# Optimization experiments

Measured on AMD Instinct MI355X. Metric: run time of the kernel, lower is better.

## Reference

```python
import jax, jax.numpy as jnp
import numpy as np

D_MODEL = 1024
N_HEADS = 16
D_HEAD = 64
D_MLP = 4096
EPS = 1e-6


def setup_inputs() -> dict:
    key = jax.random.key(0)
    ks = jax.random.split(key, 12)
    s = lambda fan_in: 1.0 / np.sqrt(fan_in)
    x = jax.random.normal(ks[0], (2, 2048, D_MODEL), dtype=jnp.float32)
    inp = {
        "x": x,
        "ln1_w": jnp.ones((D_MODEL,), jnp.float32),
        "ln2_w": jnp.ones((D_MODEL,), jnp.float32),
        "Wq": jax.random.normal(ks[1], (D_MODEL, N_HEADS * D_HEAD), jnp.float32) * s(D_MODEL),
        "bq": jnp.zeros((N_HEADS * D_HEAD,), jnp.float32),
        "Wk": jax.random.normal(ks[2], (D_MODEL, N_HEADS * D_HEAD), jnp.float32) * s(D_MODEL),
        "bk": jnp.zeros((N_HEADS * D_HEAD,), jnp.float32),
        "Wv": jax.random.normal(ks[3], (D_MODEL, N_HEADS * D_HEAD), jnp.float32) * s(D_MODEL),
        "bv": jnp.zeros((N_HEADS * D_HEAD,), jnp.float32),
        "Wo": jax.random.normal(ks[4], (N_HEADS * D_HEAD, D_MODEL), jnp.float32) * s(N_HEADS * D_HEAD),
        "bo": jnp.zeros((D_MODEL,), jnp.float32),
        "Wup": jax.random.normal(ks[5], (D_MODEL, D_MLP), jnp.float32) * s(D_MODEL),
        "bup": jnp.zeros((D_MLP,), jnp.float32),
        "Wdown": jax.random.normal(ks[6], (D_MLP, D_MODEL), jnp.float32) * s(D_MLP),
        "bdown": jnp.zeros((D_MODEL,), jnp.float32),
    }
    return inp


def _rmsnorm(x, w):
    xf = x.astype(jnp.float32)
    norm = jax.lax.rsqrt(jnp.mean(xf * xf, axis=-1, keepdims=True) + EPS)
    return (x * norm).astype(x.dtype) * w


def _attention(x, Wq, bq, Wk, bk, Wv, bv, Wo, bo):
    B, T, _ = x.shape
    q = (x @ Wq + bq).reshape(B, T, N_HEADS, D_HEAD)
    k = (x @ Wk + bk).reshape(B, T, N_HEADS, D_HEAD)
    v = (x @ Wv + bv).reshape(B, T, N_HEADS, D_HEAD)
    # [B, H, Tq, Tk]
    attn = jnp.einsum("bqhd,bkhd->bhqk", q, k) / jnp.sqrt(jnp.float32(D_HEAD))
    causal = jnp.tril(jnp.ones((T, T), dtype=bool))
    attn = jnp.where(causal, attn, -jnp.inf)
    attn = jax.nn.softmax(attn, axis=-1)
    out = jnp.einsum("bhqk,bkhd->bqhd", attn, v).reshape(B, T, N_HEADS * D_HEAD)
    return out @ Wo + bo


def reference(x, ln1_w, ln2_w, Wq, bq, Wk, bk, Wv, bv, Wo, bo, Wup, bup, Wdown, bdown):
    x = x + _attention(_rmsnorm(x, ln1_w), Wq, bq, Wk, bk, Wv, bv, Wo, bo)
    h = _rmsnorm(x, ln2_w)
    mlp = jax.nn.gelu(h @ Wup + bup, approximate=False) @ Wdown + bdown
    return x + mlp
```

## Files before the change

kernel.cpp:

```cpp
#include <hip/hip_runtime.h>
#include <cmath>

#define DM   1024
#define HDS  16
#define DH   64
#define DMLP 4096
#define TSEQ 2048
#define NROW 4096

typedef short bf16x8 __attribute__((ext_vector_type(8)));
typedef float f32x4 __attribute__((ext_vector_type(4)));

__device__ __forceinline__ unsigned short f2bf(float f) {
  union { float f; unsigned u; } v; v.f = f;
  unsigned r = v.u + 0x7fffu + ((v.u >> 16) & 1u);
  return (unsigned short)(r >> 16);
}

__device__ __forceinline__ void gload_lds16(const void* g, void* l) {
  __builtin_amdgcn_global_load_lds(
      (const __attribute__((address_space(1))) unsigned int*)g,
      (__attribute__((address_space(3))) unsigned int*)l, 16, 0, 0);
}

__global__ __launch_bounds__(256) void tr_kernel(const float* __restrict__ in,
                                                 unsigned short* __restrict__ out,
                                                 int K, int N) {
  __shared__ unsigned short tile[32][33];
  int n0 = blockIdx.x * 32, k0 = blockIdx.y * 32;
  int tx = threadIdx.x & 31, ty = threadIdx.x >> 5;
#pragma unroll
  for (int j = 0; j < 4; ++j) {
    int k = ty + j * 8;
    tile[k][tx] = f2bf(in[(size_t)(k0 + k) * N + n0 + tx]);
  }
  __syncthreads();
#pragma unroll
  for (int j = 0; j < 4; ++j) {
    int n = ty + j * 8;
    out[(size_t)(n0 + n) * K + k0 + tx] = tile[tx][n];
  }
}

__global__ void concat3_kernel(const float* __restrict__ a, const float* __restrict__ b,
                               const float* __restrict__ c, float* __restrict__ out, int n) {
  int i = blockIdx.x * 256 + threadIdx.x;
  if (i < n) { out[i] = a[i]; out[n + i] = b[i]; out[2 * n + i] = c[i]; }
}

__global__ __launch_bounds__(256) void rmsnorm_kernel(const float* __restrict__ x,
                                                      const float* __restrict__ w,
                                                      unsigned short* __restrict__ out) {
  int row = blockIdx.x;
  int t = threadIdx.x;
  const float4* xr = (const float4*)(x + (size_t)row * DM);
  float4 v = xr[t];
  float ss = v.x * v.x + v.y * v.y + v.z * v.z + v.w * v.w;
#pragma unroll
  for (int m = 1; m < 64; m <<= 1) ss += __shfl_xor(ss, m, 64);
  __shared__ float sred[4];
  if ((t & 63) == 0) sred[t >> 6] = ss;
  __syncthreads();
  ss = sred[0] + sred[1] + sred[2] + sred[3];
  float norm = rsqrtf(ss * (1.0f / DM) + 1e-6f);
  float4 wv = ((const float4*)w)[t];
  ushort4 o;
  o.x = f2bf(v.x * norm * wv.x);
  o.y = f2bf(v.y * norm * wv.y);
  o.z = f2bf(v.z * norm * wv.z);
  o.w = f2bf(v.w * norm * wv.w);
  ((ushort4*)out)[(size_t)row * (DM / 4) + t] = o;
}

template <int EPI>
__global__ __launch_bounds__(256) void gemm_bt(const unsigned short* __restrict__ A,
                                               const unsigned short* __restrict__ BT,
                                               const float* __restrict__ bias,
                                               const float* __restrict__ res,
                                               void* __restrict__ outp,
                                               int M, int N, int K) {
  __shared__ alignas(16) unsigned short As[2][128 * 32];
  __shared__ alignas(16) unsigned short Bs[2][128 * 32];
  int tid = threadIdx.x;
  int w = tid >> 6, l = tid & 63;
  unsigned nx = gridDim.x;
  unsigned bidl = blockIdx.y * nx + blockIdx.x;
  unsigned nwg = nx * gridDim.y;
  unsigned cpx = nwg >> 3;
  unsigned sb = (bidl & 7) * cpx + (bidl >> 3);
  int m0 = (int)(sb / nx) * 128, n0 = (int)(sb % nx) * 128;
  int wr = w >> 1, wc = w & 1;
  f32x4 acc[4][4];
#pragma unroll
  for (int i = 0; i < 4; ++i)
#pragma unroll
    for (int j = 0; j < 4; ++j)
#pragma unroll
      for (int e = 0; e < 4; ++e) acc[i][j][e] = 0.0f;

  int nk = K >> 5;
  int arow = tid >> 2, aslot = tid & 3;

#define STG128(BUF, KT)                                                            \
  {                                                                                \
    _Pragma("unroll") for (int i = 0; i < 2; ++i) {                                \
      int row = i * 64 + arow;                                                     \
      gload_lds16(A + (size_t)(m0 + row) * K + (size_t)(KT) * 32 + aslot * 8,      \
                  (char*)As[BUF] + i * 4096 + w * 1024);                           \
      gload_lds16(BT + (size_t)(n0 + row) * K + (size_t)(KT) * 32 + aslot * 8,     \
                  (char*)Bs[BUF] + i * 4096 + w * 1024);                           \
    }                                                                              \
  }

  STG128(0, 0);
  __syncthreads();
  int cur = 0;
  for (int kt = 0; kt < nk; ++kt) {
    if (kt + 1 < nk) STG128(cur ^ 1, kt + 1);
    bf16x8 af[4], bfr[4];
#pragma unroll
    for (int mt = 0; mt < 4; ++mt)
      af[mt] = *(const bf16x8*)((const char*)As[cur] +
                (size_t)(wr * 64 + mt * 16 + (l & 15)) * 64 + (l >> 4) * 16);
#pragma unroll
    for (int nt = 0; nt < 4; ++nt)
      bfr[nt] = *(const bf16x8*)((const char*)Bs[cur] +
                 (size_t)(wc * 64 + nt * 16 + (l & 15)) * 64 + (l >> 4) * 16);
#pragma unroll
    for (int mt = 0; mt < 4; ++mt)
#pragma unroll
      for (int nt = 0; nt < 4; ++nt)
        acc[mt][nt] = __builtin_amdgcn_mfma_f32_16x16x32_bf16(af[mt], bfr[nt], acc[mt][nt], 0, 0, 0);
    __syncthreads();
    cur ^= 1;
  }
#undef STG128

  int g = l >> 4, c = l & 15;
#pragma unroll
  for (int mt = 0; mt < 4; ++mt) {
#pragma unroll
    for (int nt = 0; nt < 4; ++nt) {
#pragma unroll
      for (int r = 0; r < 4; ++r) {
        int m = m0 + wr * 64 + mt * 16 + g * 4 + r;
        int n = n0 + wc * 64 + nt * 16 + c;
        float v = acc[mt][nt][r] + bias[n];
        if (EPI == 2) v = 0.5f * v * (1.0f + erff(v * 0.70710678118654752f));
        if (EPI == 1) {
          v += res[(size_t)m * N + n];
          ((float*)outp)[(size_t)m * N + n] = v;
        } else {
          ((unsigned short*)outp)[(size_t)m * N + n] = f2bf(v);
        }
      }
    }
  }
}

template <int EPI>
__global__ __launch_bounds__(512) void gemm_db256(const unsigned short* __restrict__ A,
                                                  const unsigned short* __restrict__ BT,
                                                  const float* __restrict__ bias,
                                                  const float* __restrict__ res,
                                                  void* __restrict__ outp,
                                                  int M, int N, int K) {
  __shared__ alignas(16) unsigned short As[2][256 * 64];
  __shared__ alignas(16) unsigned short Bs[2][256 * 64];
  int tid = threadIdx.x;
  int w = tid >> 6, l = tid & 63;
  int wr = w >> 2, wc = w & 3;
  unsigned nx = gridDim.x;
  unsigned bidl = blockIdx.y * nx + blockIdx.x;
  unsigned nwg = nx * gridDim.y;
  unsigned cpx = nwg >> 3;
  unsigned sb = (bidl & 7) * cpx + (bidl >> 3);
  int m0 = (int)(sb / nx) * 256, n0 = (int)(sb % nx) * 256;

  f32x4 acc[8][4];
#pragma unroll
  for (int i = 0; i < 8; ++i)
#pragma unroll
    for (int j = 0; j < 4; ++j)
#pragma unroll
      for (int e = 0; e < 4; ++e) acc[i][j][e] = 0.0f;

  int nk = K >> 6;
  int srow = tid >> 3, sslot = tid & 7;
  int gslot = sslot ^ (srow & 7);
  int c = l & 15, g = l >> 4;

#define STG256(BUF, KT)                                                            \
  {                                                                                \
    _Pragma("unroll") for (int i = 0; i < 4; ++i) {                                \
      int row = i * 64 + srow;                                                     \
      gload_lds16(A + (size_t)(m0 + row) * K + (size_t)(KT) * 64 + gslot * 8,      \
                  (char*)As[BUF] + i * 8192 + w * 1024);                           \
      gload_lds16(BT + (size_t)(n0 + row) * K + (size_t)(KT) * 64 + gslot * 8,     \
                  (char*)Bs[BUF] + i * 8192 + w * 1024);                           \
    }                                                                              \
  }

  STG256(0, 0);
  __syncthreads();
  int cur = 0;
  for (int kt = 0; kt < nk; ++kt) {
    if (kt + 1 < nk) STG256(cur ^ 1, kt + 1);
#pragma unroll
    for (int ks = 0; ks < 2; ++ks) {
      bf16x8 bfr[4];
#pragma unroll
      for (int nt = 0; nt < 4; ++nt) {
        int brow = wc * 64 + nt * 16 + c;
        unsigned bslot = (unsigned)((ks * 4 + g) ^ (brow & 7));
        bfr[nt] = *(const bf16x8*)((const char*)Bs[cur] + (size_t)brow * 128 + bslot * 16);
      }
#pragma unroll
      for (int mt = 0; mt < 8; ++mt) {
        int arow2 = wr * 128 + mt * 16 + c;
        unsigned aslot2 = (unsigned)((ks * 4 + g) ^ (arow2 & 7));
        bf16x8 af = *(const bf16x8*)((const char*)As[cur] + (size_t)arow2 * 128 + aslot2 * 16);
#pragma unroll
        for (int nt = 0; nt < 4; ++nt)
          acc[mt][nt] = __builtin_amdgcn_mfma_f32_16x16x32_bf16(af, bfr[nt], acc[mt][nt], 0, 0, 0);
      }
    }
    __syncthreads();
    cur ^= 1;
  }
#undef STG256

#pragma unroll
  for (int mt = 0; mt < 8; ++mt) {
#pragma unroll
    for (int nt = 0; nt < 4; ++nt) {
#pragma unroll
      for (int r = 0; r < 4; ++r) {
        int m = m0 + wr * 128 + mt * 16 + g * 4 + r;
        int n = n0 + wc * 64 + nt * 16 + c;
        float v = acc[mt][nt][r] + bias[n];
        if (EPI == 2) v = 0.5f * v * (1.0f + erff(v * 0.70710678118654752f));
        if (EPI == 1) {
          v += res[(size_t)m * N + n];
          ((float*)outp)[(size_t)m * N + n] = v;
        } else {
          ((unsigned short*)outp)[(size_t)m * N + n] = f2bf(v);
        }
      }
    }
  }
}

__global__ __launch_bounds__(256) void vtr_kernel(const unsigned short* __restrict__ qkv,
                                                  unsigned short* __restrict__ vt) {
  __shared__ unsigned short tile[64][72];
  int bh = blockIdx.y, t0 = blockIdx.x * 64;
  int b = bh >> 4, h = bh & 15;
  int r = threadIdx.x >> 3, sl = threadIdx.x & 7;
#pragma unroll
  for (int half = 0; half < 2; ++half) {
    int rr = r + half * 32;
    bf16x8 v = *(const bf16x8*)(qkv + (size_t)(b * TSEQ + t0 + rr) * 3072 + 2048 + h * 64 + sl * 8);
    *(bf16x8*)&tile[rr][sl * 8] = v;
  }
  __syncthreads();
#pragma unroll
  for (int half = 0; half < 2; ++half) {
    int d = r + half * 32;
    bf16x8 o;
#pragma unroll
    for (int j = 0; j < 8; ++j) o[j] = (short)tile[sl * 8 + j][d];
    *(bf16x8*)(vt + ((size_t)bh * 64 + d) * TSEQ + t0 + sl * 8) = o;
  }
}

__global__ __launch_bounds__(256) void attn_kernel(const unsigned short* __restrict__ qkv,
                                                   const unsigned short* __restrict__ vt,
                                                   unsigned short* __restrict__ attn_out) {
  __shared__ alignas(16) unsigned short Ks[2][64 * 64];
  __shared__ alignas(16) unsigned short Vs[2][64 * 64];
  __shared__ alignas(16) unsigned short Ps[4][2][16 * 64];
  int tid = threadIdx.x, w = tid >> 6, l = tid & 63, g = l >> 4, c = l & 15;
  int bid = blockIdx.x;
  int pair = bid & 15;
  int bh = bid >> 4, b = bh >> 4, h = bh & 15;
  int qbh = 31 - pair, qbl = pair;
  int qwh = qbh * 64 + w * 16;
  int qwl = qbl * 64 + w * 16;

  bf16x8 qfh[2], qfl[2];
#pragma unroll
  for (int s = 0; s < 2; ++s) {
    qfh[s] = *(const bf16x8*)(qkv + (size_t)(b * TSEQ + qwh + c) * 3072 + h * 64 + s * 32 + g * 8);
    qfl[s] = *(const bf16x8*)(qkv + (size_t)(b * TSEQ + qwl + c) * 3072 + h * 64 + s * 32 + g * 8);
  }

  f32x4 oh[4], ol[4];
  float mh[4], lh[4], ml[4], ll[4];
#pragma unroll
  for (int dc = 0; dc < 4; ++dc)
#pragma unroll
    for (int e = 0; e < 4; ++e) { oh[dc][e] = 0.0f; ol[dc][e] = 0.0f; }
#pragma unroll
  for (int r = 0; r < 4; ++r) { mh[r] = -1e30f; lh[r] = 0.0f; ml[r] = -1e30f; ll[r] = 0.0f; }

  int ntile = qbh + 1;
  int sr = tid >> 3, ss = tid & 7;
  bf16x8 kreg[2], vreg[2];

#define LOADT(K0)                                                                       \
  {                                                                                     \
    _Pragma("unroll") for (int hf = 0; hf < 2; ++hf) {                                  \
      int rr = sr + hf * 32;                                                            \
      kreg[hf] = *(const bf16x8*)(qkv + (size_t)(b * TSEQ + (K0) + rr) * 3072 + 1024 +  \
                                  h * 64 + ss * 8);                                     \
      vreg[hf] = *(const bf16x8*)(vt + ((size_t)bh * 64 + rr) * TSEQ + (K0) + ss * 8);  \
    }                                                                                   \
  }
#define WRITET(BUF)                                                                     \
  {                                                                                     \
    _Pragma("unroll") for (int hf = 0; hf < 2; ++hf) {                                  \
      int rr = sr + hf * 32;                                                            \
      unsigned off = (unsigned)(rr * 128 + ss * 16) ^ (unsigned)((rr & 7) << 4);        \
      *(bf16x8*)((char*)Ks[BUF] + off) = kreg[hf];                                      \
      *(bf16x8*)((char*)Vs[BUF] + off) = vreg[hf];                                      \
    }                                                                                   \
  }
#define COMPQ(QF, O, MR, LP, QW, PSL)                                                   \
  {                                                                                     \
    f32x4 s_[4];                                                                        \
    _Pragma("unroll") for (int ni = 0; ni < 4; ++ni) {                                  \
      int krow_ = ni * 16 + c;                                                          \
      unsigned swz_ = (unsigned)((c & 7) << 4);                                         \
      bf16x8 kf0_ = *(const bf16x8*)(Kb + (((unsigned)(krow_ * 128) + g * 16) ^ swz_)); \
      bf16x8 kf1_ = *(const bf16x8*)(Kb + (((unsigned)(krow_ * 128) + 64 + g * 16) ^ swz_)); \
      f32x4 a_;                                                                         \
      _Pragma("unroll") for (int e = 0; e < 4; ++e) a_[e] = 0.0f;                       \
      a_ = __builtin_amdgcn_mfma_f32_16x16x32_bf16(QF[0], kf0_, a_, 0, 0, 0);           \
      a_ = __builtin_amdgcn_mfma_f32_16x16x32_bf16(QF[1], kf1_, a_, 0, 0, 0);           \
      s_[ni] = a_;                                                                      \
    }                                                                                   \
    bool full_ = (k0 + 63 <= (QW));                                                     \
    _Pragma("unroll") for (int r = 0; r < 4; ++r) {                                     \
      int qg_ = (QW) + g * 4 + r;                                                       \
      float pm_[4];                                                                     \
      _Pragma("unroll") for (int ni = 0; ni < 4; ++ni) {                                \
        float v_ = s_[ni][r] * 0.125f;                                                  \
        if (!full_) {                                                                   \
          int kg_ = k0 + ni * 16 + c;                                                   \
          v_ = (kg_ <= qg_) ? v_ : -1e30f;                                              \
        }                                                                               \
        pm_[ni] = v_;                                                                   \
      }                                                                                 \
      float mx_ = fmaxf(fmaxf(pm_[0], pm_[1]), fmaxf(pm_[2], pm_[3]));                  \
      mx_ = fmaxf(mx_, __shfl_xor(mx_, 1, 64));                                         \
      mx_ = fmaxf(mx_, __shfl_xor(mx_, 2, 64));                                         \
      mx_ = fmaxf(mx_, __shfl_xor(mx_, 4, 64));                                         \
      mx_ = fmaxf(mx_, __shfl_xor(mx_, 8, 64));                                         \
      float mnew_ = fmaxf(MR[r], mx_);                                                  \
      float scale_ = __expf(MR[r] - mnew_);                                             \
      MR[r] = mnew_;                                                                    \
      float p_[4], rs_ = 0.0f;                                                          \
      _Pragma("unroll") for (int ni = 0; ni < 4; ++ni) {                                \
        p_[ni] = __expf(pm_[ni] - mnew_); rs_ += p_[ni];                                \
      }                                                                                 \
      LP[r] = LP[r] * scale_ + rs_;                                                     \
      _Pragma("unroll") for (int dc = 0; dc < 4; ++dc) O[dc][r] *= scale_;              \
      int prow_ = g * 4 + r;                                                            \
      unsigned pswz_ = (unsigned)((prow_ & 7) << 4);                                    \
      _Pragma("unroll") for (int ni = 0; ni < 4; ++ni)                                  \
        *(unsigned short*)((char*)Ps[w][PSL] +                                          \
            (((unsigned)(prow_ * 128 + (ni * 16 + c) * 2)) ^ pswz_)) = f2bf(p_[ni]);    \
    }                                                                                   \
    asm volatile("s_waitcnt lgkmcnt(0)" ::: "memory");                                  \
    unsigned swz2_ = (unsigned)((c & 7) << 4);                                          \
    _Pragma("unroll") for (int kc = 0; kc < 2; ++kc) {                                  \
      bf16x8 pf_ = *(const bf16x8*)((const char*)Ps[w][PSL] +                           \
                    (((unsigned)(c * 128 + kc * 64 + g * 16)) ^ swz2_));                \
      _Pragma("unroll") for (int dc = 0; dc < 4; ++dc) {                                \
        bf16x8 vf_ = *(const bf16x8*)(Vb +                                              \
                      (((unsigned)((dc * 16 + c) * 128 + kc * 64 + g * 16)) ^ swz2_));  \
        O[dc] = __builtin_amdgcn_mfma_f32_16x16x32_bf16(pf_, vf_, O[dc], 0, 0, 0);      \
      }                                                                                 \
    }                                                                                   \
  }

  LOADT(0);
  WRITET(0);
  __syncthreads();

  for (int t = 0; t < ntile; ++t) {
    int k0 = t << 6, cur = t & 1;
    if (t + 1 < ntile) LOADT((t + 1) << 6);

    {
      const char* Kb = (const char*)Ks[cur];
      const char* Vb = (const char*)Vs[cur];
      COMPQ(qfh, oh, mh, lh, qwh, 0);
      if (k0 <= qwl + 15) COMPQ(qfl, ol, ml, ll, qwl, 1);
    }

    if (t + 1 < ntile) {
      WRITET(cur ^ 1);
      __syncthreads();
    }
  }

#pragma unroll
  for (int r = 0; r < 4; ++r) {
    float lrh = lh[r], lrl = ll[r];
    lrh += __shfl_xor(lrh, 1, 64);
    lrh += __shfl_xor(lrh, 2, 64);
    lrh += __shfl_xor(lrh, 4, 64);
    lrh += __shfl_xor(lrh, 8, 64);
    lrl += __shfl_xor(lrl, 1, 64);
    lrl += __shfl_xor(lrl, 2, 64);
    lrl += __shfl_xor(lrl, 4, 64);
    lrl += __shfl_xor(lrl, 8, 64);
    float invh = 1.0f / lrh, invl = 1.0f / lrl;
    size_t rowh = (size_t)b * TSEQ + qwh + g * 4 + r;
    size_t rowl = (size_t)b * TSEQ + qwl + g * 4 + r;
    unsigned short* oph = attn_out + rowh * 1024 + h * 64 + c;
    unsigned short* opl = attn_out + rowl * 1024 + h * 64 + c;
#pragma unroll
    for (int dc = 0; dc < 4; ++dc) {
      oph[dc * 16] = f2bf(oh[dc][r] * invh);
      opl[dc * 16] = f2bf(ol[dc][r] * invl);
    }
  }
#undef LOADT
#undef WRITET
#undef COMPQ
}

extern "C" void kernel_launch(void* const* d_in, const int* in_sizes, int n_in,
                              void* d_out, int out_size, void* d_ws, size_t ws_size,
                              hipStream_t stream) {
  const float* x    = (const float*)d_in[0];
  const float* ln1w = (const float*)d_in[1];
  const float* ln2w = (const float*)d_in[2];
  const float* Wq   = (const float*)d_in[3];
  const float* bq   = (const float*)d_in[4];
  const float* Wk   = (const float*)d_in[5];
  const float* bk   = (const float*)d_in[6];
  const float* Wv   = (const float*)d_in[7];
  const float* bv   = (const float*)d_in[8];
  const float* Wo   = (const float*)d_in[9];
  const float* bo   = (const float*)d_in[10];
  const float* Wup  = (const float*)d_in[11];
  const float* bup  = (const float*)d_in[12];
  const float* Wdn  = (const float*)d_in[13];
  const float* bdn  = (const float*)d_in[14];

  char* ws = (char*)d_ws;
  unsigned short* xn1   = (unsigned short*)(ws + 0);
  unsigned short* vtb   = (unsigned short*)(ws + 0);
  unsigned short* qkv   = (unsigned short*)(ws + (8ull << 20));
  unsigned short* gbuf  = (unsigned short*)(ws + 0);
  unsigned short* attn  = (unsigned short*)(ws + (32ull << 20));
  float*          x2    = (float*)(ws + (40ull << 20));
  unsigned short* h2    = (unsigned short*)(ws + (56ull << 20));
  unsigned short* WqkvT = (unsigned short*)(ws + (64ull << 20));
  unsigned short* WoT   = (unsigned short*)(ws + (70ull << 20));
  unsigned short* WupT  = (unsigned short*)(ws + (72ull << 20));
  unsigned short* WdnT  = (unsigned short*)(ws + (80ull << 20));
  float*          bqkv  = (float*)(ws + (88ull << 20));

  dim3 blk(256);
  dim3 blk512(512);
  tr_kernel<<<dim3(32, 32), blk, 0, stream>>>(Wq, WqkvT, 1024, 1024);
  tr_kernel<<<dim3(32, 32), blk, 0, stream>>>(Wk, WqkvT + 1024 * 1024, 1024, 1024);
  tr_kernel<<<dim3(32, 32), blk, 0, stream>>>(Wv, WqkvT + 2 * 1024 * 1024, 1024, 1024);
  tr_kernel<<<dim3(32, 32), blk, 0, stream>>>(Wo, WoT, 1024, 1024);
  tr_kernel<<<dim3(128, 32), blk, 0, stream>>>(Wup, WupT, 1024, 4096);
  tr_kernel<<<dim3(32, 128), blk, 0, stream>>>(Wdn, WdnT, 4096, 1024);
  concat3_kernel<<<dim3(4), blk, 0, stream>>>(bq, bk, bv, bqkv, 1024);

  rmsnorm_kernel<<<dim3(NROW), blk, 0, stream>>>(x, ln1w, xn1);
  gemm_db256<0><<<dim3(12, 16), blk512, 0, stream>>>(xn1, WqkvT, bqkv, nullptr, qkv, NROW, 3072, 1024);

  vtr_kernel<<<dim3(32, 32), blk, 0, stream>>>(qkv, vtb);
  attn_kernel<<<dim3(512), blk, 0, stream>>>(qkv, vtb, attn);

  gemm_bt<1><<<dim3(8, 32), blk, 0, stream>>>(attn, WoT, bo, x, x2, NROW, 1024, 1024);

  rmsnorm_kernel<<<dim3(NROW), blk, 0, stream>>>(x2, ln2w, h2);
  gemm_db256<2><<<dim3(16, 16), blk512, 0, stream>>>(h2, WupT, bup, nullptr, gbuf, NROW, 4096, 1024);
  gemm_bt<1><<<dim3(8, 32), blk, 0, stream>>>(gbuf, WdnT, bdn, x2, d_out, NROW, 1024, 4096);
}
```

Measured before the change: 418.2 us.

## Split-K the down-projection GEMM and widen gemm_bt K-tile with swizzled LDS

The down-projection GEMM (K=4096) is split into two K halves on a z grid dimension. Each half writes fp32 partials to workspace, and a separate reduce kernel adds the partials, bias and residual. This is meant to double the number of workgroups on a 256-tile launch that underfills the device. gemm_bt also moves to a 64-wide K tile with XOR-swizzled LDS slots to cut barrier count and LDS bank conflicts. The cost is extra fp32 partial traffic and one more kernel launch, and the split path only runs when the workspace is at least 128MB.

```diff
diff --git a/kernel.cpp b/kernel.cpp
--- a/kernel.cpp
+++ b/kernel.cpp
@@ -72,15 +72,32 @@
   ((ushort4*)out)[(size_t)row * (DM / 4) + t] = o;
 }
 
+__global__ __launch_bounds__(256) void reduce_sk(const float* __restrict__ part,
+                                                 const float* __restrict__ bias,
+                                                 const float* __restrict__ res,
+                                                 float* __restrict__ out, int MN, int N) {
+  size_t i = (size_t)blockIdx.x * 256 + threadIdx.x;
+  const float4* p0 = (const float4*)part;
+  const float4* p1 = p0 + (MN >> 2);
+  float4 a = p0[i], b = p1[i], r = ((const float4*)res)[i];
+  float4 bi = ((const float4*)bias)[i & ((N >> 2) - 1)];
+  float4 o;
+  o.x = a.x + b.x + r.x + bi.x;
+  o.y = a.y + b.y + r.y + bi.y;
+  o.z = a.z + b.z + r.z + bi.z;
+  o.w = a.w + b.w + r.w + bi.w;
+  ((float4*)out)[i] = o;
+}
+
 template <int EPI>
 __global__ __launch_bounds__(256) void gemm_bt(const unsigned short* __restrict__ A,
                                                const unsigned short* __restrict__ BT,
                                                const float* __restrict__ bias,
                                                const float* __restrict__ res,
                                                void* __restrict__ outp,
-                                               int M, int N, int K) {
-  __shared__ alignas(16) unsigned short As[2][128 * 32];
-  __shared__ alignas(16) unsigned short Bs[2][128 * 32];
+                                               int M, int N, int K, int klen) {
+  __shared__ alignas(16) unsigned short As[2][128 * 64];
+  __shared__ alignas(16) unsigned short Bs[2][128 * 64];
   int tid = threadIdx.x;
   int w = tid >> 6, l = tid & 63;
   unsigned nx = gridDim.x;
@@ -90,6 +107,7 @@
   unsigned sb = (bidl & 7) * cpx + (bidl >> 3);
   int m0 = (int)(sb / nx) * 128, n0 = (int)(sb % nx) * 128;
   int wr = w >> 1, wc = w & 1;
+  int kbase = (int)blockIdx.z * klen;
   f32x4 acc[4][4];
 #pragma unroll
   for (int i = 0; i < 4; ++i)
@@ -98,16 +116,18 @@
 #pragma unroll
       for (int e = 0; e < 4; ++e) acc[i][j][e] = 0.0f;
 
-  int nk = K >> 5;
-  int arow = tid >> 2, aslot = tid & 3;
+  int nk = klen >> 6;
+  int srow = tid >> 3;
+  int gslot = (tid & 7) ^ (srow & 7);
+  int c = l & 15, g = l >> 4;
 
 #define STG128(BUF, KT)                                                            \
   {                                                                                \
-    _Pragma("unroll") for (int i = 0; i < 2; ++i) {                                \
-      int row = i * 64 + arow;                                                     \
-      gload_lds16(A + (size_t)(m0 + row) * K + (size_t)(KT) * 32 + aslot * 8,      \
+    _Pragma("unroll") for (int i = 0; i < 4; ++i) {                                \
+      int row = i * 32 + srow;                                                     \
+      gload_lds16(A + (size_t)(m0 + row) * K + kbase + (size_t)(KT) * 64 + gslot * 8, \
                   (char*)As[BUF] + i * 4096 + w * 1024);                           \
-      gload_lds16(BT + (size_t)(n0 + row) * K + (size_t)(KT) * 32 + aslot * 8,     \
+      gload_lds16(BT + (size_t)(n0 + row) * K + kbase + (size_t)(KT) * 64 + gslot * 8, \
                   (char*)Bs[BUF] + i * 4096 + w * 1024);                           \
     }                                                                              \
   }
@@ -117,26 +137,31 @@
   int cur = 0;
   for (int kt = 0; kt < nk; ++kt) {
     if (kt + 1 < nk) STG128(cur ^ 1, kt + 1);
-    bf16x8 af[4], bfr[4];
-#pragma unroll
-    for (int mt = 0; mt < 4; ++mt)
-      af[mt] = *(const bf16x8*)((const char*)As[cur] +
-                (size_t)(wr * 64 + mt * 16 + (l & 15)) * 64 + (l >> 4) * 16);
-#pragma unroll
-    for (int nt = 0; nt < 4; ++nt)
-      bfr[nt] = *(const bf16x8*)((const char*)Bs[cur] +
-                 (size_t)(wc * 64 + nt * 16 + (l & 15)) * 64 + (l >> 4) * 16);
-#pragma unroll
-    for (int mt = 0; mt < 4; ++mt)
-#pragma unroll
-      for (int nt = 0; nt < 4; ++nt)
-        acc[mt][nt] = __builtin_amdgcn_mfma_f32_16x16x32_bf16(af[mt], bfr[nt], acc[mt][nt], 0, 0, 0);
+#pragma unroll
+    for (int ks = 0; ks < 2; ++ks) {
+      bf16x8 bfr[4];
+#pragma unroll
+      for (int nt = 0; nt < 4; ++nt) {
+        int brow = wc * 64 + nt * 16 + c;
+        unsigned bslot = (unsigned)((ks * 4 + g) ^ (brow & 7));
+        bfr[nt] = *(const bf16x8*)((const char*)Bs[cur] + (size_t)brow * 128 + bslot * 16);
+      }
+#pragma unroll
+      for (int mt = 0; mt < 4; ++mt) {
+        int arow2 = wr * 64 + mt * 16 + c;
+        unsigned aslot2 = (unsigned)((ks * 4 + g) ^ (arow2 & 7));
+        bf16x8 af = *(const bf16x8*)((const char*)As[cur] + (size_t)arow2 * 128 + aslot2 * 16);
+#pragma unroll
+        for (int nt = 0; nt < 4; ++nt)
+          acc[mt][nt] = __builtin_amdgcn_mfma_f32_16x16x32_bf16(af, bfr[nt], acc[mt][nt], 0, 0, 0);
+      }
+    }
     __syncthreads();
     cur ^= 1;
   }
 #undef STG128
 
-  int g = l >> 4, c = l & 15;
+  float* po = (float*)outp + (size_t)blockIdx.z * M * N;
 #pragma unroll
   for (int mt = 0; mt < 4; ++mt) {
 #pragma unroll
@@ -145,13 +170,12 @@
       for (int r = 0; r < 4; ++r) {
         int m = m0 + wr * 64 + mt * 16 + g * 4 + r;
         int n = n0 + wc * 64 + nt * 16 + c;
-        float v = acc[mt][nt][r] + bias[n];
-        if (EPI == 2) v = 0.5f * v * (1.0f + erff(v * 0.70710678118654752f));
+        float v = acc[mt][nt][r];
         if (EPI == 1) {
-          v += res[(size_t)m * N + n];
+          v += bias[n] + res[(size_t)m * N + n];
           ((float*)outp)[(size_t)m * N + n] = v;
         } else {
-          ((unsigned short*)outp)[(size_t)m * N + n] = f2bf(v);
+          po[(size_t)m * N + n] = v;
         }
       }
     }
@@ -465,6 +489,9 @@
   unsigned short* WupT  = (unsigned short*)(ws + (72ull << 20));
   unsigned short* WdnT  = (unsigned short*)(ws + (80ull << 20));
   float*          bqkv  = (float*)(ws + (88ull << 20));
+  float*          part  = (float*)(ws + (96ull << 20));
+
+  bool sk = ws_size >= (128ull << 20);
 
   dim3 blk(256);
   dim3 blk512(512);
@@ -482,9 +509,15 @@
   vtr_kernel<<<dim3(32, 32), blk, 0, stream>>>(qkv, vtb);
   attn_kernel<<<dim3(512), blk, 0, stream>>>(qkv, vtb, attn);
 
-  gemm_bt<1><<<dim3(8, 32), blk, 0, stream>>>(attn, WoT, bo, x, x2, NROW, 1024, 1024);
+  gemm_bt<1><<<dim3(8, 32), blk, 0, stream>>>(attn, WoT, bo, x, x2, NROW, 1024, 1024, 1024);
 
   rmsnorm_kernel<<<dim3(NROW), blk, 0, stream>>>(x2, ln2w, h2);
   gemm_db256<2><<<dim3(16, 16), blk512, 0, stream>>>(h2, WupT, bup, nullptr, gbuf, NROW, 4096, 1024);
-  gemm_bt<1><<<dim3(8, 32), blk, 0, stream>>>(gbuf, WdnT, bdn, x2, d_out, NROW, 1024, 4096);
-}
+  if (sk) {
+    gemm_bt<3><<<dim3(8, 32, 2), blk, 0, stream>>>(gbuf, WdnT, nullptr, nullptr, part,
+                                                   NROW, 1024, 4096, 2048);
+    reduce_sk<<<dim3(4096), blk, 0, stream>>>(part, bdn, x2, (float*)d_out, NROW * 1024, 1024);
+  } else {
+    gemm_bt<1><<<dim3(8, 32), blk, 0, stream>>>(gbuf, WdnT, bdn, x2, d_out, NROW, 1024, 4096, 4096);
+  }
+}
```

Result: faster. 390.4 us (-6.6%).
